# Performance work log

Hardware: AMD Instinct MI355X
Metric: run time of the kernel (lower is better)

The kernel has to match this reference:

```python
import jax, jax.numpy as jnp
import numpy as np

S, B, F = 2048, 2, 1024
H, D = 16, 64
P = H * D  # packed dim = 1024


def setup_inputs() -> dict:
    key = jax.random.key(0)
    k1, k2, k3 = jax.random.split(key, 3)
    return {
        "src": jax.random.normal(k1, (S, B, F), dtype=jnp.float32),
        "in_proj_weight": jax.random.normal(k2, (3 * P, F), dtype=jnp.float32) * (1.0 / np.sqrt(F)),
        "in_proj_bias": jnp.zeros((3 * P,), dtype=jnp.float32),
        "out_proj_weight": jax.random.normal(k3, (F, P), dtype=jnp.float32) * (1.0 / np.sqrt(P)),
        "out_proj_bias": jnp.zeros((F,), dtype=jnp.float32),
    }


def reference(src, in_proj_weight, in_proj_bias, out_proj_weight, out_proj_bias):
    s, b, f = src.shape
    h, d = H, D
    # fused QKV projection: [S,B,3P]
    qkv = jnp.einsum("sbf,pf->sbp", src, in_proj_weight) + in_proj_bias
    q, k, v = jnp.split(qkv, 3, axis=-1)  # each [S,B,P]
    # [S,B,P] -> [S, B*H, D] -> [B*H, S, D]
    def to_heads(x):
        return jnp.swapaxes(x.reshape(s, b * h, d), 0, 1)
    q = to_heads(q) / np.sqrt(d)
    k = to_heads(k)
    v = to_heads(v)
    attn = jnp.einsum("nsd,ntd->nst", q, k)  # [B*H, S, S]
    attn = jax.nn.softmax(attn, axis=-1)
    out = jnp.einsum("nst,ntd->nsd", attn, v)  # [B*H, S, D]
    out = jnp.swapaxes(out, 0, 1).reshape(s * b, h * d)  # [S*B, P]
    out = out @ out_proj_weight.T + out_proj_bias  # [S*B, F]
    return out.reshape(s, b, f)
```

## Files before the change

kernel.cpp:

```cpp
#include <hip/hip_runtime.h>

#define S_LEN 2048
#define B_SZ  2
#define F_DIM 1024
#define H_N   16
#define D_DIM 64
#define P_DIM 1024
#define M_ROWS 4096
#define NBH   32

typedef __bf16 bf16x8 __attribute__((ext_vector_type(8)));
typedef __bf16 bf16x4 __attribute__((ext_vector_type(4)));
typedef float  f32x4  __attribute__((ext_vector_type(4)));
typedef unsigned short u16;
typedef unsigned short u16x8 __attribute__((ext_vector_type(8)));
typedef unsigned short u16x4 __attribute__((ext_vector_type(4)));

__device__ __forceinline__ float bf2f(u16 u) {
  union { unsigned int i; float f; } x;
  x.i = ((unsigned int)u) << 16;
  return x.f;
}
__device__ __forceinline__ u16 f2bf(float f) {
  union { float f; unsigned int i; } x;
  x.f = f;
  unsigned int u = x.i;
  u += 0x7fffu + ((u >> 16) & 1u);
  return (u16)(u >> 16);
}

__global__ __launch_bounds__(256) void cvt_all(const float* __restrict__ a,
                                               const float* __restrict__ b,
                                               const float* __restrict__ c_,
                                               u16* __restrict__ oa,
                                               u16* __restrict__ ob,
                                               u16* __restrict__ oc) {
  int i = blockIdx.x * 256 + threadIdx.x;
  const float* in;
  u16* out;
  int off;
  if (i < 1048576)      { in = a;  out = oa; off = i; }
  else if (i < 1835008) { in = b;  out = ob; off = i - 1048576; }
  else                  { in = c_; out = oc; off = i - 1835008; }
  f32x4 v = *reinterpret_cast<const f32x4*>(in + (size_t)off * 4);
  u16x4 o;
  o[0] = f2bf(v[0]); o[1] = f2bf(v[1]); o[2] = f2bf(v[2]); o[3] = f2bf(v[3]);
  *reinterpret_cast<u16x4*>(out + (size_t)off * 4) = o;
}

__device__ __forceinline__ void stage_tile(const u16* __restrict__ gbase,
                                           u16* lds, int row0, int k0,
                                           int wave, int lane) {
  #pragma unroll
  for (int i = 0; i < 2; i++) {
    const u16* g = gbase + ((size_t)(row0 + i * 64 + wave * 16 + (lane >> 2)) << 10)
                 + k0 + (lane & 3) * 8;
    u16* l = lds + (i * 64 + wave * 16) * 32;
    __builtin_amdgcn_global_load_lds(
        (const __attribute__((address_space(1))) void*)(const void*)g,
        (__attribute__((address_space(3))) void*)(void*)l, 16, 0, 0);
  }
}

__global__ __launch_bounds__(256) void qkv_gemm(const u16* __restrict__ A,
                                                const u16* __restrict__ W,
                                                const float* __restrict__ bias,
                                                u16* __restrict__ qw,
                                                u16* __restrict__ kw,
                                                u16* __restrict__ vt) {
  __shared__ u16 As[3][128 * 32];
  __shared__ u16 Bs[3][128 * 32];

  const int lane = threadIdx.x & 63;
  const int wave = threadIdx.x >> 6;
  const int wr = wave >> 1, wc = wave & 1;
  const int bm = blockIdx.y * 128;
  const int bn = blockIdx.x * 128;
  const int c = lane & 15;
  const int g = lane >> 4;

  f32x4 acc[4][4];
  #pragma unroll
  for (int mi = 0; mi < 4; mi++)
    #pragma unroll
    for (int ni = 0; ni < 4; ni++) {
      f32x4 z = {0.f, 0.f, 0.f, 0.f};
      acc[mi][ni] = z;
    }

  stage_tile(A, As[0], bm, 0, wave, lane);
  stage_tile(W, Bs[0], bn, 0, wave, lane);
  stage_tile(A, As[1], bm, 32, wave, lane);
  stage_tile(W, Bs[1], bn, 32, wave, lane);

  int cur = 0;
  for (int kt = 0; kt < 32; kt++) {
    if (kt < 31) asm volatile("s_waitcnt vmcnt(4)" ::: "memory");
    else         asm volatile("s_waitcnt vmcnt(0)" ::: "memory");
    __builtin_amdgcn_s_barrier();
    __builtin_amdgcn_sched_barrier(0);
    if (kt + 2 < 32) {
      int nb = cur + 2; if (nb >= 3) nb -= 3;
      stage_tile(A, As[nb], bm, (kt + 2) * 32, wave, lane);
      stage_tile(W, Bs[nb], bn, (kt + 2) * 32, wave, lane);
    }
    bf16x8 a[4], b[4];
    #pragma unroll
    for (int mi = 0; mi < 4; mi++)
      a[mi] = *reinterpret_cast<const bf16x8*>(&As[cur][(wr * 64 + mi * 16 + c) * 32 + g * 8]);
    #pragma unroll
    for (int ni = 0; ni < 4; ni++)
      b[ni] = *reinterpret_cast<const bf16x8*>(&Bs[cur][(wc * 64 + ni * 16 + c) * 32 + g * 8]);
    __builtin_amdgcn_s_setprio(1);
    #pragma unroll
    for (int mi = 0; mi < 4; mi++)
      #pragma unroll
      for (int ni = 0; ni < 4; ni++)
        acc[mi][ni] = __builtin_amdgcn_mfma_f32_16x16x32_bf16(a[mi], b[ni], acc[mi][ni], 0, 0, 0);
    __builtin_amdgcn_s_setprio(0);
    cur = (cur == 2) ? 0 : cur + 1;
  }

  const int which = bn >> 10;
  const float qscale = 0.125f * 1.44269504f;
  #pragma unroll
  for (int ni = 0; ni < 4; ni++) {
    const int p = bn + wc * 64 + ni * 16 + c;
    const float bv = bias[p];
    const int pp = p & 1023;
    const int h = pp >> 6, d = pp & 63;
    #pragma unroll
    for (int mi = 0; mi < 4; mi++) {
      #pragma unroll
      for (int r = 0; r < 4; r++) {
        const int m = bm + wr * 64 + mi * 16 + g * 4 + r;
        const int s = m >> 1, b_ = m & 1;
        const int n = b_ * 16 + h;
        if (which == 0)
          qw[((size_t)n * 2048 + s) * 64 + d] = f2bf((acc[mi][ni][r] + bv) * qscale);
        else if (which == 1)
          kw[((size_t)n * 2048 + s) * 64 + d] = f2bf(acc[mi][ni][r] + bv);
        else
          vt[((size_t)n * 64 + d) * 2048 + s] = f2bf(acc[mi][ni][r] + bv);
      }
    }
  }
}

__global__ __launch_bounds__(256) void out_gemm(const u16* __restrict__ A,
                                                const u16* __restrict__ W,
                                                const float* __restrict__ bias,
                                                float* __restrict__ out) {
  __shared__ u16 As[3][128 * 32];
  __shared__ u16 Bs[3][128 * 32];

  const int lane = threadIdx.x & 63;
  const int wave = threadIdx.x >> 6;
  const int wr = wave >> 1, wc = wave & 1;
  const int bm = blockIdx.y * 128;
  const int bn = blockIdx.x * 128;
  const int c = lane & 15;
  const int g = lane >> 4;

  f32x4 acc[4][4];
  #pragma unroll
  for (int mi = 0; mi < 4; mi++)
    #pragma unroll
    for (int ni = 0; ni < 4; ni++) {
      f32x4 z = {0.f, 0.f, 0.f, 0.f};
      acc[mi][ni] = z;
    }

  stage_tile(A, As[0], bm, 0, wave, lane);
  stage_tile(W, Bs[0], bn, 0, wave, lane);
  stage_tile(A, As[1], bm, 32, wave, lane);
  stage_tile(W, Bs[1], bn, 32, wave, lane);

  int cur = 0;
  for (int kt = 0; kt < 32; kt++) {
    if (kt < 31) asm volatile("s_waitcnt vmcnt(4)" ::: "memory");
    else         asm volatile("s_waitcnt vmcnt(0)" ::: "memory");
    __builtin_amdgcn_s_barrier();
    __builtin_amdgcn_sched_barrier(0);
    if (kt + 2 < 32) {
      int nb = cur + 2; if (nb >= 3) nb -= 3;
      stage_tile(A, As[nb], bm, (kt + 2) * 32, wave, lane);
      stage_tile(W, Bs[nb], bn, (kt + 2) * 32, wave, lane);
    }
    bf16x8 a[4], b[4];
    #pragma unroll
    for (int mi = 0; mi < 4; mi++)
      a[mi] = *reinterpret_cast<const bf16x8*>(&As[cur][(wr * 64 + mi * 16 + c) * 32 + g * 8]);
    #pragma unroll
    for (int ni = 0; ni < 4; ni++)
      b[ni] = *reinterpret_cast<const bf16x8*>(&Bs[cur][(wc * 64 + ni * 16 + c) * 32 + g * 8]);
    __builtin_amdgcn_s_setprio(1);
    #pragma unroll
    for (int mi = 0; mi < 4; mi++)
      #pragma unroll
      for (int ni = 0; ni < 4; ni++)
        acc[mi][ni] = __builtin_amdgcn_mfma_f32_16x16x32_bf16(a[mi], b[ni], acc[mi][ni], 0, 0, 0);
    __builtin_amdgcn_s_setprio(0);
    cur = (cur == 2) ? 0 : cur + 1;
  }

  #pragma unroll
  for (int ni = 0; ni < 4; ni++) {
    const int f = bn + wc * 64 + ni * 16 + c;
    const float bv = bias[f];
    #pragma unroll
    for (int mi = 0; mi < 4; mi++) {
      #pragma unroll
      for (int r = 0; r < 4; r++) {
        const int m = bm + wr * 64 + mi * 16 + g * 4 + r;
        out[(size_t)m * 1024 + f] = acc[mi][ni][r] + bv;
      }
    }
  }
}

__device__ __forceinline__ void stage_kv(const u16* __restrict__ kb,
                                         const u16* __restrict__ vb,
                                         int ks0, u16* ksbuf, u16* vsbuf,
                                         int wave, int tid) {
  #pragma unroll
  for (int i = 0; i < 2; i++) {
    const int chunk = i * 256 + tid;
    const int row = chunk >> 3;
    const int scc = (chunk & 7) ^ (row & 7);
    u16* lk = ksbuf + (i * 256 + wave * 64) * 8;
    u16* lv = vsbuf + (i * 256 + wave * 64) * 8;
    __builtin_amdgcn_global_load_lds(
        (const __attribute__((address_space(1))) void*)(const void*)
            (kb + (size_t)(ks0 + row) * 64 + scc * 8),
        (__attribute__((address_space(3))) void*)(void*)lk, 16, 0, 0);
    __builtin_amdgcn_global_load_lds(
        (const __attribute__((address_space(1))) void*)(const void*)
            (vb + (size_t)row * 2048 + ks0 + scc * 8),
        (__attribute__((address_space(3))) void*)(void*)lv, 16, 0, 0);
  }
}

__global__ __launch_bounds__(256) void attn_fwd(const u16* __restrict__ qw,
                                                const u16* __restrict__ kw,
                                                const u16* __restrict__ vt,
                                                u16* __restrict__ ao) {
  __shared__ u16 Ks[3][64 * 64];
  __shared__ u16 Vs[3][64 * 64];
  __shared__ u16 Pl[4][32][76];

  const int tid = threadIdx.x;
  const int wave = tid >> 6;
  const int lane = tid & 63;
  const int c = lane & 15;
  const int g = lane >> 4;
  const int sw = c & 7;

  const int bid = blockIdx.x;
  const int id = (bid & 7) * 64 + (bid >> 3);
  const int n = id >> 4;
  const int qt = id & 15;
  const int b_ = n >> 4, h = n & 15;
  const int q0 = qt * 128 + wave * 32;

  bf16x8 qb[2][2];
  #pragma unroll
  for (int sp = 0; sp < 2; sp++)
    #pragma unroll
    for (int kk = 0; kk < 2; kk++)
      qb[sp][kk] = *reinterpret_cast<const bf16x8*>(
          qw + ((size_t)n * 2048 + q0 + sp * 16 + c) * 64 + kk * 32 + g * 8);

  const u16* kb = kw + (size_t)n * 2048 * 64;
  const u16* vb = vt + (size_t)n * 64 * 2048;

  f32x4 O[2][4];
  float l_run[2] = {0.f, 0.f};
  #pragma unroll
  for (int sp = 0; sp < 2; sp++)
    #pragma unroll
    for (int dt = 0; dt < 4; dt++) {
      f32x4 z = {0.f, 0.f, 0.f, 0.f};
      O[sp][dt] = z;
    }

  stage_kv(kb, vb, 0,  Ks[0], Vs[0], wave, tid);
  stage_kv(kb, vb, 64, Ks[1], Vs[1], wave, tid);

  int cur = 0;
  for (int kt = 0; kt < 32; kt++) {
    if (kt < 31) asm volatile("s_waitcnt vmcnt(4)" ::: "memory");
    else         asm volatile("s_waitcnt vmcnt(0)" ::: "memory");
    __builtin_amdgcn_s_barrier();
    __builtin_amdgcn_sched_barrier(0);
    if (kt + 2 < 32) {
      int nb = cur + 2; if (nb >= 3) nb -= 3;
      stage_kv(kb, vb, (kt + 2) * 64, Ks[nb], Vs[nb], wave, tid);
    }

    f32x4 s[2][4];
    #pragma unroll
    for (int sp = 0; sp < 2; sp++)
      #pragma unroll
      for (int st = 0; st < 4; st++) { f32x4 z = {0.f,0.f,0.f,0.f}; s[sp][st] = z; }
    __builtin_amdgcn_s_setprio(1);
    #pragma unroll
    for (int st = 0; st < 4; st++) {
      #pragma unroll
      for (int kk = 0; kk < 2; kk++) {
        bf16x8 ka = *reinterpret_cast<const bf16x8*>(
            &Ks[cur][(st * 16 + c) * 64 + ((kk * 4 + g) ^ sw) * 8]);
        s[0][st] = __builtin_amdgcn_mfma_f32_16x16x32_bf16(ka, qb[0][kk], s[0][st], 0, 0, 0);
        s[1][st] = __builtin_amdgcn_mfma_f32_16x16x32_bf16(ka, qb[1][kk], s[1][st], 0, 0, 0);
      }
    }
    __builtin_amdgcn_s_setprio(0);

    #pragma unroll
    for (int sp = 0; sp < 2; sp++) {
      float psum = 0.f;
      #pragma unroll
      for (int st = 0; st < 4; st++) {
        const float p0 = __builtin_amdgcn_exp2f(s[sp][st][0]);
        const float p1 = __builtin_amdgcn_exp2f(s[sp][st][1]);
        const float p2 = __builtin_amdgcn_exp2f(s[sp][st][2]);
        const float p3 = __builtin_amdgcn_exp2f(s[sp][st][3]);
        psum += (p0 + p1) + (p2 + p3);
        bf16x4 pk = { (__bf16)p0, (__bf16)p1, (__bf16)p2, (__bf16)p3 };
        *reinterpret_cast<bf16x4*>(&Pl[wave][sp * 16 + c][st * 16 + g * 4]) = pk;
      }
      l_run[sp] += psum;
    }

    __builtin_amdgcn_s_setprio(1);
    #pragma unroll
    for (int kk = 0; kk < 2; kk++) {
      bf16x8 pa0 = *reinterpret_cast<const bf16x8*>(&Pl[wave][ 0 + c][kk * 32 + g * 8]);
      bf16x8 pa1 = *reinterpret_cast<const bf16x8*>(&Pl[wave][16 + c][kk * 32 + g * 8]);
      #pragma unroll
      for (int dt = 0; dt < 4; dt++) {
        bf16x8 vf = *reinterpret_cast<const bf16x8*>(
            &Vs[cur][(dt * 16 + c) * 64 + ((kk * 4 + g) ^ sw) * 8]);
        O[0][dt] = __builtin_amdgcn_mfma_f32_16x16x32_bf16(pa0, vf, O[0][dt], 0, 0, 0);
        O[1][dt] = __builtin_amdgcn_mfma_f32_16x16x32_bf16(pa1, vf, O[1][dt], 0, 0, 0);
      }
    }
    __builtin_amdgcn_s_setprio(0);

    cur = (cur == 2) ? 0 : cur + 1;
  }

  #pragma unroll
  for (int sp = 0; sp < 2; sp++) {
    float lt = l_run[sp];
    lt += __shfl_xor(lt, 16);
    lt += __shfl_xor(lt, 32);
    #pragma unroll
    for (int r = 0; r < 4; r++) {
      const float lq = __shfl(lt, g * 4 + r);
      const float inv = 1.0f / lq;
      const int q = q0 + sp * 16 + g * 4 + r;
      const size_t m = (size_t)q * 2 + b_;
      #pragma unroll
      for (int dt = 0; dt < 4; dt++)
        ao[m * 1024 + h * 64 + dt * 16 + c] = f2bf(O[sp][dt][r] * inv);
    }
  }
}

extern "C" void kernel_launch(void* const* d_in, const int* in_sizes, int n_in,
                              void* d_out, int out_size, void* d_ws, size_t ws_size,
                              hipStream_t stream) {
  const float* src   = (const float*)d_in[0];
  const float* w_in  = (const float*)d_in[1];
  const float* b_in  = (const float*)d_in[2];
  const float* w_out = (const float*)d_in[3];
  const float* b_out = (const float*)d_in[4];
  float* out = (float*)d_out;

  char* ws = (char*)d_ws;
  u16* srcb = (u16*)(ws);
  u16* wib  = (u16*)(ws + ((size_t)8  << 20));
  u16* wob  = (u16*)(ws + ((size_t)14 << 20));
  u16* qw   = (u16*)(ws + ((size_t)16 << 20));
  u16* kw   = (u16*)(ws + ((size_t)24 << 20));
  u16* vt   = (u16*)(ws + ((size_t)32 << 20));
  u16* ao   = (u16*)(ws + ((size_t)40 << 20));

  cvt_all<<<8192, 256, 0, stream>>>(src, w_in, w_out, srcb, wib, wob);

  qkv_gemm<<<dim3(24, 32), 256, 0, stream>>>(srcb, wib, b_in, qw, kw, vt);
  attn_fwd<<<512, 256, 0, stream>>>(qw, kw, vt, ao);
  out_gemm<<<dim3(8, 32), 256, 0, stream>>>(ao, wob, b_out, out);
}
```

Measured before the change: 131.7 us.

## Switch attention to 32x32x16 MFMA and keep P in registers via permlane swap

```diff
diff --git a/kernel.cpp b/kernel.cpp
--- a/kernel.cpp
+++ b/kernel.cpp
@@ -12,6 +12,7 @@
 typedef __bf16 bf16x8 __attribute__((ext_vector_type(8)));
 typedef __bf16 bf16x4 __attribute__((ext_vector_type(4)));
 typedef float  f32x4  __attribute__((ext_vector_type(4)));
+typedef float  f32x16 __attribute__((ext_vector_type(16)));
 typedef unsigned short u16;
 typedef unsigned short u16x8 __attribute__((ext_vector_type(8)));
 typedef unsigned short u16x4 __attribute__((ext_vector_type(4)));
@@ -247,14 +248,12 @@
                                                 u16* __restrict__ ao) {
   __shared__ u16 Ks[3][64 * 64];
   __shared__ u16 Vs[3][64 * 64];
-  __shared__ u16 Pl[4][32][76];
 
   const int tid = threadIdx.x;
   const int wave = tid >> 6;
   const int lane = tid & 63;
-  const int c = lane & 15;
-  const int g = lane >> 4;
-  const int sw = c & 7;
+  const int qc = lane & 31;
+  const int hi = lane >> 5;
 
   const int bid = blockIdx.x;
   const int id = (bid & 7) * 64 + (bid >> 3);
@@ -263,26 +262,21 @@
   const int b_ = n >> 4, h = n & 15;
   const int q0 = qt * 128 + wave * 32;
 
-  bf16x8 qb[2][2];
-  #pragma unroll
-  for (int sp = 0; sp < 2; sp++)
-    #pragma unroll
-    for (int kk = 0; kk < 2; kk++)
-      qb[sp][kk] = *reinterpret_cast<const bf16x8*>(
-          qw + ((size_t)n * 2048 + q0 + sp * 16 + c) * 64 + kk * 32 + g * 8);
+  bf16x8 qb[4];
+  #pragma unroll
+  for (int ks = 0; ks < 4; ks++)
+    qb[ks] = *reinterpret_cast<const bf16x8*>(
+        qw + ((size_t)n * 2048 + q0 + qc) * 64 + ks * 16 + hi * 8);
 
   const u16* kb = kw + (size_t)n * 2048 * 64;
   const u16* vb = vt + (size_t)n * 64 * 2048;
 
-  f32x4 O[2][4];
-  float l_run[2] = {0.f, 0.f};
-  #pragma unroll
-  for (int sp = 0; sp < 2; sp++)
-    #pragma unroll
-    for (int dt = 0; dt < 4; dt++) {
-      f32x4 z = {0.f, 0.f, 0.f, 0.f};
-      O[sp][dt] = z;
-    }
+  f32x16 O[2];
+  #pragma unroll
+  for (int dh = 0; dh < 2; dh++)
+    #pragma unroll
+    for (int r = 0; r < 16; r++) O[dh][r] = 0.f;
+  float l_run = 0.f;
 
   stage_kv(kb, vb, 0,  Ks[0], Vs[0], wave, tid);
   stage_kv(kb, vb, 64, Ks[1], Vs[1], wave, tid);
@@ -298,72 +292,75 @@
       stage_kv(kb, vb, (kt + 2) * 64, Ks[nb], Vs[nb], wave, tid);
     }
 
-    f32x4 s[2][4];
-    #pragma unroll
-    for (int sp = 0; sp < 2; sp++)
-      #pragma unroll
-      for (int st = 0; st < 4; st++) { f32x4 z = {0.f,0.f,0.f,0.f}; s[sp][st] = z; }
-    __builtin_amdgcn_s_setprio(1);
-    #pragma unroll
-    for (int st = 0; st < 4; st++) {
-      #pragma unroll
-      for (int kk = 0; kk < 2; kk++) {
+    #pragma unroll
+    for (int kh = 0; kh < 2; kh++) {
+      f32x16 s;
+      #pragma unroll
+      for (int r = 0; r < 16; r++) s[r] = 0.f;
+      const int krow = kh * 32 + qc;
+      __builtin_amdgcn_s_setprio(1);
+      #pragma unroll
+      for (int ks = 0; ks < 4; ks++) {
         bf16x8 ka = *reinterpret_cast<const bf16x8*>(
-            &Ks[cur][(st * 16 + c) * 64 + ((kk * 4 + g) ^ sw) * 8]);
-        s[0][st] = __builtin_amdgcn_mfma_f32_16x16x32_bf16(ka, qb[0][kk], s[0][st], 0, 0, 0);
-        s[1][st] = __builtin_amdgcn_mfma_f32_16x16x32_bf16(ka, qb[1][kk], s[1][st], 0, 0, 0);
-      }
-    }
-    __builtin_amdgcn_s_setprio(0);
-
-    #pragma unroll
-    for (int sp = 0; sp < 2; sp++) {
+            &Ks[cur][krow * 64 + (((ks * 2 + hi) ^ (qc & 7)) * 8)]);
+        s = __builtin_amdgcn_mfma_f32_32x32x16_bf16(ka, qb[ks], s, 0, 0, 0);
+      }
+      __builtin_amdgcn_s_setprio(0);
+
+      float p[16];
       float psum = 0.f;
       #pragma unroll
-      for (int st = 0; st < 4; st++) {
-        const float p0 = __builtin_amdgcn_exp2f(s[sp][st][0]);
-        const float p1 = __builtin_amdgcn_exp2f(s[sp][st][1]);
-        const float p2 = __builtin_amdgcn_exp2f(s[sp][st][2]);
-        const float p3 = __builtin_amdgcn_exp2f(s[sp][st][3]);
-        psum += (p0 + p1) + (p2 + p3);
-        bf16x4 pk = { (__bf16)p0, (__bf16)p1, (__bf16)p2, (__bf16)p3 };
-        *reinterpret_cast<bf16x4*>(&Pl[wave][sp * 16 + c][st * 16 + g * 4]) = pk;
-      }
-      l_run[sp] += psum;
-    }
-
-    __builtin_amdgcn_s_setprio(1);
-    #pragma unroll
-    for (int kk = 0; kk < 2; kk++) {
-      bf16x8 pa0 = *reinterpret_cast<const bf16x8*>(&Pl[wave][ 0 + c][kk * 32 + g * 8]);
-      bf16x8 pa1 = *reinterpret_cast<const bf16x8*>(&Pl[wave][16 + c][kk * 32 + g * 8]);
-      #pragma unroll
-      for (int dt = 0; dt < 4; dt++) {
-        bf16x8 vf = *reinterpret_cast<const bf16x8*>(
-            &Vs[cur][(dt * 16 + c) * 64 + ((kk * 4 + g) ^ sw) * 8]);
-        O[0][dt] = __builtin_amdgcn_mfma_f32_16x16x32_bf16(pa0, vf, O[0][dt], 0, 0, 0);
-        O[1][dt] = __builtin_amdgcn_mfma_f32_16x16x32_bf16(pa1, vf, O[1][dt], 0, 0, 0);
-      }
-    }
-    __builtin_amdgcn_s_setprio(0);
+      for (int r = 0; r < 16; r++) { p[r] = __builtin_amdgcn_exp2f(s[r]); psum += p[r]; }
+      l_run += psum;
+
+      unsigned u[8];
+      #pragma unroll
+      for (int r1 = 0; r1 < 4; r1++) {
+        asm("v_cvt_pk_bf16_f32 %0, %1, %2" : "=v"(u[2 * r1])     : "v"(p[4 * r1 + 0]), "v"(p[4 * r1 + 1]));
+        asm("v_cvt_pk_bf16_f32 %0, %1, %2" : "=v"(u[2 * r1 + 1]) : "v"(p[4 * r1 + 2]), "v"(p[4 * r1 + 3]));
+      }
+      asm("v_permlane32_swap_b32 %0, %1" : "+v"(u[0]), "+v"(u[2]));
+      asm("v_permlane32_swap_b32 %0, %1" : "+v"(u[1]), "+v"(u[3]));
+      asm("v_permlane32_swap_b32 %0, %1" : "+v"(u[4]), "+v"(u[6]));
+      asm("v_permlane32_swap_b32 %0, %1" : "+v"(u[5]), "+v"(u[7]));
+      union AF { unsigned w[4]; bf16x8 v; };
+      AF af0, af1;
+      af0.w[0] = u[0]; af0.w[1] = u[1]; af0.w[2] = u[2]; af0.w[3] = u[3];
+      af1.w[0] = u[4]; af1.w[1] = u[5]; af1.w[2] = u[6]; af1.w[3] = u[7];
+
+      __builtin_amdgcn_s_setprio(1);
+      #pragma unroll
+      for (int ks2 = 0; ks2 < 2; ks2++) {
+        #pragma unroll
+        for (int dh = 0; dh < 2; dh++) {
+          const int dr = dh * 32 + qc;
+          bf16x8 vf = *reinterpret_cast<const bf16x8*>(
+              &Vs[cur][dr * 64 + ((((kh * 2 + ks2) * 2 + hi) ^ (qc & 7)) * 8)]);
+          O[dh] = __builtin_amdgcn_mfma_f32_32x32x16_bf16(ks2 ? af1.v : af0.v, vf, O[dh], 0, 0, 0);
+        }
+      }
+      __builtin_amdgcn_s_setprio(0);
+    }
 
     cur = (cur == 2) ? 0 : cur + 1;
   }
 
-  #pragma unroll
-  for (int sp = 0; sp < 2; sp++) {
-    float lt = l_run[sp];
-    lt += __shfl_xor(lt, 16);
-    lt += __shfl_xor(lt, 32);
-    #pragma unroll
-    for (int r = 0; r < 4; r++) {
-      const float lq = __shfl(lt, g * 4 + r);
-      const float inv = 1.0f / lq;
-      const int q = q0 + sp * 16 + g * 4 + r;
+  l_run += __shfl_xor(l_run, 32);
+
+  float inv16[16];
+  #pragma unroll
+  for (int r = 0; r < 16; r++) {
+    const int qrow = (r & 3) + 8 * (r >> 2) + 4 * hi;
+    inv16[r] = 1.0f / __shfl(l_run, qrow);
+  }
+  #pragma unroll
+  for (int dh = 0; dh < 2; dh++) {
+    #pragma unroll
+    for (int r = 0; r < 16; r++) {
+      const int qrow = (r & 3) + 8 * (r >> 2) + 4 * hi;
+      const int q = q0 + qrow;
       const size_t m = (size_t)q * 2 + b_;
-      #pragma unroll
-      for (int dt = 0; dt < 4; dt++)
-        ao[m * 1024 + h * 64 + dt * 16 + c] = f2bf(O[sp][dt][r] * inv);
+      ao[m * 1024 + h * 64 + dh * 32 + qc] = f2bf(O[dh][r] * inv16[r]);
     }
   }
 }
```

Result: no change. 129.4 us (-1.7%).
